# Kernel optimization log

Hardware: AMD Instinct MI355X
Metric: run time of the kernel (lower is better)

The kernel has to match this reference:

```python
import jax, jax.numpy as jnp
import numpy as np

B, T, E, H, DH = 8, 1024, 1024, 16, 64

def setup_inputs() -> dict:
    key = jax.random.key(0)
    ks = jax.random.split(key, 5)
    x = jax.random.normal(ks[0], (B, T, E), dtype=jnp.float32)
    Wq = jax.random.normal(ks[1], (H, E, DH), dtype=jnp.float32) * (E ** -0.5)
    Wk = jax.random.normal(ks[2], (H, E, DH), dtype=jnp.float32) * (E ** -0.5)
    Wv = jax.random.normal(ks[3], (H, E, DH), dtype=jnp.float32) * (E ** -0.5)
    Wp = jax.random.normal(ks[4], (E, E), dtype=jnp.float32) * (E ** -0.5)
    bp = jnp.zeros((E,), dtype=jnp.float32)
    return {"x": x, "Wq": Wq, "Wk": Wk, "Wv": Wv, "Wp": Wp, "bp": bp}

def reference(x, Wq, Wk, Wv, Wp, bp):
    # per-head projections (bias-free), vectorized over heads
    q = jnp.einsum('bte,hed->bhtd', x, Wq)
    k = jnp.einsum('bte,hed->bhtd', x, Wk)
    v = jnp.einsum('bte,hed->bhtd', x, Wv)
    scale = DH ** -0.5
    att = jnp.einsum('bhtd,bhsd->bhts', q, k) * scale  # [B,H,T,T]
    causal = jnp.tril(jnp.ones((T, T), dtype=bool))
    att = jnp.where(causal, att, -jnp.inf)
    att = jax.nn.softmax(att, axis=-1)
    # dropout is identity in eval mode
    out = jnp.einsum('bhts,bhsd->bhtd', att, v)
    out = out.transpose(0, 2, 1, 3).reshape(B, T, E)  # concat heads in order
    # proj: torch Linear y = x @ W^T + b
    out = out @ Wp.T + bp
    return out
```

## Files before the change

### kernel.cpp

```cpp
#include <hip/hip_runtime.h>

#define Bsz 8
#define Tsz 1024
#define Esz 1024
#define Hsz 16
#define DHsz 64
#define NQKV 3072

typedef _Float16 f16x8 __attribute__((ext_vector_type(8)));
typedef float f32x4 __attribute__((ext_vector_type(4)));
typedef unsigned short u16x8 __attribute__((ext_vector_type(8)));

__device__ __forceinline__ unsigned short f2h(float f) {
    union { _Float16 h; unsigned short u; } cv;
    cv.h = (_Float16)f;
    return cv.u;
}

__device__ __forceinline__ void async16(const void* g, void* l) {
    __builtin_amdgcn_global_load_lds(
        (const __attribute__((address_space(1))) void*)g,
        (__attribute__((address_space(3))) void*)l, 16, 0, 0);
}

#define MFMA(a, b, c) __builtin_amdgcn_mfma_f32_16x16x32_f16((a), (b), (c), 0, 0, 0)


__global__ void cast_f16_kernel(const float* __restrict__ in, unsigned short* __restrict__ outp) {
    int i = (blockIdx.x * 256 + threadIdx.x) * 4;
    float4 v = *(const float4*)(in + i);
    ushort4 o;
    o.x = f2h(v.x); o.y = f2h(v.y); o.z = f2h(v.z); o.w = f2h(v.w);
    *(ushort4*)(outp + i) = o;
}

__global__ void pack_wqkv_kernel(const float* __restrict__ Wq, const float* __restrict__ Wk,
                                 const float* __restrict__ Wv, unsigned short* __restrict__ Bt) {
    int i = (blockIdx.x * 256 + threadIdx.x) * 4;
    int n = i >> 10;
    int e = i & 1023;
    int which = n >> 10, rem = n & 1023, h = rem >> 6, d = rem & 63;
    const float* W = (which == 0) ? Wq : ((which == 1) ? Wk : Wv);
    const float* src = W + ((size_t)h * Esz + e) * DHsz + d;
    ushort4 o;
    o.x = f2h(src[0]);
    o.y = f2h(src[DHsz]);
    o.z = f2h(src[2 * DHsz]);
    o.w = f2h(src[3 * DHsz]);
    *(ushort4*)(Bt + i) = o;
}

__global__ __launch_bounds__(256) void vtrans_kernel(const unsigned short* __restrict__ QKV,
                                                     unsigned short* __restrict__ VT) {
    __shared__ unsigned int tile[64 * 33];
    const int bh = blockIdx.x, tc = blockIdx.y;
    const int b = bh >> 4, h = bh & 15;
    const int tid = threadIdx.x;
    const unsigned short* src = QKV + ((size_t)(b * Tsz) + tc * 64) * NQKV + 2048 + h * 64;
#pragma unroll
    for (int it = 0; it < 2; ++it) {
        int task = tid + it * 256;
        int row = task >> 3, seg = task & 7;
        u16x8 v = *(const u16x8*)(src + (size_t)row * NQKV + seg * 8);
#pragma unroll
        for (int jj = 0; jj < 4; ++jj)
            tile[row * 33 + seg * 4 + jj] =
                (unsigned int)v[2 * jj] | ((unsigned int)v[2 * jj + 1] << 16);
    }
    __syncthreads();
    unsigned short* dst = VT + (size_t)bh * DHsz * Tsz + tc * 64;
#pragma unroll
    for (int it = 0; it < 2; ++it) {
        int task = tid + it * 256;
        int d = task & 63, tseg = task >> 6;
        int du = d >> 1, hi = d & 1;
        u16x8 v;
#pragma unroll
        for (int j = 0; j < 8; ++j) {
            unsigned int w = tile[(tseg * 8 + j) * 33 + du];
            v[j] = (unsigned short)(hi ? (w >> 16) : (w & 0xffffu));
        }
        *(u16x8*)(dst + (size_t)d * Tsz + tseg * 8) = v;
    }
}

template <int MODE>
__global__ __launch_bounds__(256, 3) void gemm_bt(
    const unsigned short* __restrict__ A,
    const unsigned short* __restrict__ Bt,
    int K, int N,
    unsigned short* __restrict__ c16,
    float* __restrict__ outp, const float* __restrict__ bias)
{
    __shared__ unsigned short smem[17408];
    unsigned short* sA = smem;
    unsigned short* sB = smem + 4096;
    const int tid = threadIdx.x;
    const int wid = tid >> 6, lane = tid & 63;
    const int quad = lane >> 4, l16 = lane & 15;
    const int col0 = blockIdx.x * 128;
    const int row0 = blockIdx.y * 128;
    const int wm = (wid >> 1) * 64, wn = (wid & 1) * 64;

    const f32x4 zero4 = {0.f, 0.f, 0.f, 0.f};
    f32x4 acc[4][4];
#pragma unroll
    for (int i = 0; i < 4; ++i)
#pragma unroll
        for (int j = 0; j < 4; ++j) acc[i][j] = zero4;

    const unsigned short* gA = A + (size_t)row0 * K;
    const unsigned short* gB = Bt + (size_t)col0 * K;
    const int c0 = wid * 2;
    const int srw = lane >> 2;
    const int ssg = (lane & 3) * 8;

    for (int k0 = 0; k0 < K; k0 += 32) {
#pragma unroll
        for (int cc = 0; cc < 2; ++cc) {
            int c = c0 + cc;
            async16(gA + (size_t)(c * 16 + srw) * K + k0 + ssg, (void*)(sA + c * 512 + lane * 8));
            async16(gB + (size_t)(c * 16 + srw) * K + k0 + ssg, (void*)(sB + c * 512 + lane * 8));
        }
        __syncthreads();

        f16x8 af[4], bfr[4];
#pragma unroll
        for (int i = 0; i < 4; ++i)
            af[i] = *(const f16x8*)(sA + (wm + i * 16 + l16) * 32 + quad * 8);
#pragma unroll
        for (int j = 0; j < 4; ++j)
            bfr[j] = *(const f16x8*)(sB + (wn + j * 16 + l16) * 32 + quad * 8);
#pragma unroll
        for (int i = 0; i < 4; ++i)
#pragma unroll
            for (int j = 0; j < 4; ++j)
                acc[i][j] = MFMA(af[i], bfr[j], acc[i][j]);
        __syncthreads();
    }

    if (MODE == 0) {
#pragma unroll
        for (int i = 0; i < 4; ++i)
#pragma unroll
            for (int r = 0; r < 4; ++r) {
                int rowL = wm + i * 16 + quad * 4 + r;
                unsigned short* tr = smem + rowL * 136 + wn + l16;
#pragma unroll
                for (int j = 0; j < 4; ++j)
                    tr[j * 16] = f2h(acc[i][j][r]);
            }
        __syncthreads();
        unsigned short* ob = c16 + (size_t)row0 * N + col0;
#pragma unroll
        for (int it = 0; it < 8; ++it) {
            int rowG = wid * 32 + it * 4 + quad;
            u16x8 v = *(const u16x8*)(smem + rowG * 136 + l16 * 8);
            *(u16x8*)(ob + (size_t)rowG * N + l16 * 8) = v;
        }
    } else {
#pragma unroll
        for (int i = 0; i < 4; ++i) {
            int rb = row0 + wm + i * 16 + quad * 4;
#pragma unroll
            for (int r = 0; r < 4; ++r) {
                float* orow = outp + (size_t)(rb + r) * N;
#pragma unroll
                for (int j = 0; j < 4; ++j) {
                    int c = col0 + wn + j * 16 + l16;
                    orow[c] = acc[i][j][r] + bias[c];
                }
            }
        }
    }
}

__global__ __launch_bounds__(256, 4) void attn_kernel(
    const unsigned short* __restrict__ QKV,
    const unsigned short* __restrict__ VTg,
    unsigned short* __restrict__ AO)
{
    const int bh = blockIdx.x;
    const int qt = 7 - blockIdx.y;
    const int b = bh >> 4, h = bh & 15;
    const int q0 = qt * 128;
    const int tid = threadIdx.x, wid = tid >> 6, lane = tid & 63;
    const int quad = lane >> 4, l16 = lane & 15;

    __shared__ unsigned short sK[64 * 64];
    __shared__ unsigned short sVt[64 * 64];
    __shared__ unsigned short sP[128 * 72];

    const unsigned short* Qb = QKV + (size_t)(b * Tsz) * NQKV + h * 64;
    const unsigned short* Kb = QKV + (size_t)(b * Tsz) * NQKV + 1024 + h * 64;
    const unsigned short* VTb = VTg + (size_t)bh * DHsz * Tsz;

    const int srow = lane >> 3;
    const int sseg = lane & 7;
    const int slog = sseg ^ srow;

    const float C1 = 0.18033688f;
    const float C2 = -4.32808512f;
    const f32x4 zero4 = {0.f, 0.f, 0.f, 0.f};

    const int rowlo = q0 + wid * 32;
    const int prow0 = wid * 32;

    f16x8 qf[2][2];
#pragma unroll
    for (int rt = 0; rt < 2; ++rt)
#pragma unroll
        for (int kk = 0; kk < 2; ++kk)
            qf[rt][kk] = *(const f16x8*)(Qb + (size_t)(rowlo + rt * 16 + l16) * NQKV +
                                         kk * 32 + quad * 8);

    f32x4 o[2][4];
    float lp[2][4];
#pragma unroll
    for (int rt = 0; rt < 2; ++rt) {
#pragma unroll
        for (int dt = 0; dt < 4; ++dt) o[rt][dt] = zero4;
#pragma unroll
        for (int r = 0; r < 4; ++r) lp[rt][r] = 0.f;
    }

    const int nblk = (q0 >> 6) + 2;
    for (int blk = 0; blk < nblk; ++blk) {
        const int s0 = blk * 64;
        __syncthreads();
        {
            const int r0 = wid * 16;
#pragma unroll
            for (int ii = 0; ii < 2; ++ii) {
                int rr = r0 + ii * 8;
                async16(Kb + (size_t)(s0 + rr + srow) * NQKV + slog * 8,
                        (void*)(sK + rr * 64 + lane * 8));
                async16(VTb + (size_t)(rr + srow) * Tsz + s0 + slog * 8,
                        (void*)(sVt + rr * 64 + lane * 8));
            }
        }
        __syncthreads();

        if (s0 > rowlo + 31) continue;

        f32x4 sc[2][4];
#pragma unroll
        for (int rt = 0; rt < 2; ++rt)
#pragma unroll
            for (int ct = 0; ct < 4; ++ct) sc[rt][ct] = zero4;
#pragma unroll
        for (int kk = 0; kk < 2; ++kk) {
            f16x8 kf[4];
#pragma unroll
            for (int ct = 0; ct < 4; ++ct)
                kf[ct] = *(const f16x8*)(sK + (ct * 16 + l16) * 64 +
                                         (((kk * 4 + quad) ^ (l16 & 7)) * 8));
#pragma unroll
            for (int rt = 0; rt < 2; ++rt)
#pragma unroll
                for (int ct = 0; ct < 4; ++ct)
                    sc[rt][ct] = MFMA(qf[rt][kk], kf[ct], sc[rt][ct]);
        }

        if (s0 + 63 <= rowlo) {
#pragma unroll
            for (int rt = 0; rt < 2; ++rt)
#pragma unroll
                for (int r = 0; r < 4; ++r) {
                    unsigned short* pr = sP + (prow0 + rt * 16 + quad * 4 + r) * 72 + l16;
#pragma unroll
                    for (int ct = 0; ct < 4; ++ct) {
                        float p = exp2f(fmaf(sc[rt][ct][r], C1, C2));
                        lp[rt][r] += p;
                        pr[ct * 16] = f2h(p);
                    }
                }
        } else {
#pragma unroll
            for (int rt = 0; rt < 2; ++rt)
#pragma unroll
                for (int r = 0; r < 4; ++r) {
                    int qrow = rowlo + rt * 16 + quad * 4 + r;
                    unsigned short* pr = sP + (prow0 + rt * 16 + quad * 4 + r) * 72 + l16;
#pragma unroll
                    for (int ct = 0; ct < 4; ++ct) {
                        float p = exp2f(fmaf(sc[rt][ct][r], C1, C2));
                        p = (s0 + ct * 16 + l16 > qrow) ? 0.f : p;
                        lp[rt][r] += p;
                        pr[ct * 16] = f2h(p);
                    }
                }
        }

#pragma unroll
        for (int kk = 0; kk < 2; ++kk) {
            f16x8 pf[2], vf[4];
#pragma unroll
            for (int rt = 0; rt < 2; ++rt)
                pf[rt] = *(const f16x8*)(sP + (prow0 + rt * 16 + l16) * 72 +
                                         kk * 32 + quad * 8);
#pragma unroll
            for (int dt = 0; dt < 4; ++dt)
                vf[dt] = *(const f16x8*)(sVt + (dt * 16 + l16) * 64 +
                                         (((kk * 4 + quad) ^ (l16 & 7)) * 8));
#pragma unroll
            for (int rt = 0; rt < 2; ++rt)
#pragma unroll
                for (int dt = 0; dt < 4; ++dt)
                    o[rt][dt] = MFMA(pf[rt], vf[dt], o[rt][dt]);
        }
    }

#pragma unroll
    for (int rt = 0; rt < 2; ++rt)
#pragma unroll
        for (int r = 0; r < 4; ++r) {
            float s = lp[rt][r];
            s += __shfl_xor(s, 1, 64);
            s += __shfl_xor(s, 2, 64);
            s += __shfl_xor(s, 4, 64);
            s += __shfl_xor(s, 8, 64);
            float inv = 1.0f / s;
            int t = rowlo + rt * 16 + quad * 4 + r;
            size_t base = ((size_t)(b * Tsz + t)) * Esz + h * DHsz;
#pragma unroll
            for (int dt = 0; dt < 4; ++dt)
                AO[base + dt * 16 + l16] = f2h(o[rt][dt][r] * inv);
        }
}


extern "C" void kernel_launch(void* const* d_in, const int* in_sizes, int n_in,
                              void* d_out, int out_size, void* d_ws, size_t ws_size,
                              hipStream_t stream)
{
    const float* x  = (const float*)d_in[0];
    const float* Wq = (const float*)d_in[1];
    const float* Wk = (const float*)d_in[2];
    const float* Wv = (const float*)d_in[3];
    const float* Wp = (const float*)d_in[4];
    const float* bp = (const float*)d_in[5];
    float* out = (float*)d_out;

    char* ws = (char*)d_ws;
    unsigned short* xb   = (unsigned short*)(ws);
    unsigned short* wqkv = (unsigned short*)(ws + 16777216);
    unsigned short* wpb  = (unsigned short*)(ws + 23068672);
    unsigned short* qkv  = (unsigned short*)(ws + 25165824);
    unsigned short* ao   = (unsigned short*)(ws + 75497472);
    unsigned short* vtb  = xb;

    cast_f16_kernel<<<8192, 256, 0, stream>>>(x, xb);
    pack_wqkv_kernel<<<3072, 256, 0, stream>>>(Wq, Wk, Wv, wqkv);
    cast_f16_kernel<<<1024, 256, 0, stream>>>(Wp, wpb);

    gemm_bt<0><<<dim3(24, 64), 256, 0, stream>>>(xb, wqkv, 1024, 3072,
                                                 qkv, nullptr, nullptr);

    vtrans_kernel<<<dim3(128, 16), 256, 0, stream>>>(qkv, vtb);

    attn_kernel<<<dim3(128, 8), 256, 0, stream>>>(qkv, vtb, ao);

    gemm_bt<1><<<dim3(8, 64), 256, 0, stream>>>(ao, wpb, 1024, 1024,
                                                nullptr, out, bp);
}
```

Before: 294.8 us.

## Pair causal query tiles per block with 8 waves and staged output stores

The attention kernel now launches 512-thread blocks, and each block processes a pair of query tiles (7-p and p) one after the other, so every block does a balanced amount of causal work. Each wave now owns 16 query rows instead of 32, which lowers per-wave register use but halves the reuse of each K/V fragment loaded from LDS. The output tile is staged through shared memory and written with 16-byte vector stores instead of scattered 2-byte stores. The trade-offs are fewer blocks in total and twice as many block-wide barriers per block.

```diff
diff --git a/kernel.cpp b/kernel.cpp
--- a/kernel.cpp
+++ b/kernel.cpp
@@ -175,15 +175,14 @@
     }
 }
 
-__global__ __launch_bounds__(256, 4) void attn_kernel(
+__global__ __launch_bounds__(512, 4) void attn_kernel(
     const unsigned short* __restrict__ QKV,
     const unsigned short* __restrict__ VTg,
     unsigned short* __restrict__ AO)
 {
     const int bh = blockIdx.x;
-    const int qt = 7 - blockIdx.y;
+    const int pair = blockIdx.y;
     const int b = bh >> 4, h = bh & 15;
-    const int q0 = qt * 128;
     const int tid = threadIdx.x, wid = tid >> 6, lane = tid & 63;
     const int quad = lane >> 4, l16 = lane & 15;
 
@@ -198,135 +197,118 @@
     const int srow = lane >> 3;
     const int sseg = lane & 7;
     const int slog = sseg ^ srow;
+    const int r0 = wid * 8;
 
     const float C1 = 0.18033688f;
     const float C2 = -4.32808512f;
     const f32x4 zero4 = {0.f, 0.f, 0.f, 0.f};
 
-    const int rowlo = q0 + wid * 32;
-    const int prow0 = wid * 32;
-
-    f16x8 qf[2][2];
-#pragma unroll
-    for (int rt = 0; rt < 2; ++rt)
+    for (int half = 0; half < 2; ++half) {
+        const int qt = (half == 0) ? (7 - pair) : pair;
+        const int q0 = qt * 128;
+        const int rowlo = q0 + wid * 16;
+        const int prow0 = wid * 16;
+
+        f16x8 qf[2];
 #pragma unroll
         for (int kk = 0; kk < 2; ++kk)
-            qf[rt][kk] = *(const f16x8*)(Qb + (size_t)(rowlo + rt * 16 + l16) * NQKV +
-                                         kk * 32 + quad * 8);
-
-    f32x4 o[2][4];
-    float lp[2][4];
-#pragma unroll
-    for (int rt = 0; rt < 2; ++rt) {
-#pragma unroll
-        for (int dt = 0; dt < 4; ++dt) o[rt][dt] = zero4;
-#pragma unroll
-        for (int r = 0; r < 4; ++r) lp[rt][r] = 0.f;
-    }
-
-    const int nblk = (q0 >> 6) + 2;
-    for (int blk = 0; blk < nblk; ++blk) {
-        const int s0 = blk * 64;
-        __syncthreads();
-        {
-            const int r0 = wid * 16;
-#pragma unroll
-            for (int ii = 0; ii < 2; ++ii) {
-                int rr = r0 + ii * 8;
-                async16(Kb + (size_t)(s0 + rr + srow) * NQKV + slog * 8,
-                        (void*)(sK + rr * 64 + lane * 8));
-                async16(VTb + (size_t)(rr + srow) * Tsz + s0 + slog * 8,
-                        (void*)(sVt + rr * 64 + lane * 8));
-            }
-        }
-        __syncthreads();
-
-        if (s0 > rowlo + 31) continue;
-
-        f32x4 sc[2][4];
-#pragma unroll
-        for (int rt = 0; rt < 2; ++rt)
-#pragma unroll
-            for (int ct = 0; ct < 4; ++ct) sc[rt][ct] = zero4;
-#pragma unroll
-        for (int kk = 0; kk < 2; ++kk) {
-            f16x8 kf[4];
-#pragma unroll
-            for (int ct = 0; ct < 4; ++ct)
-                kf[ct] = *(const f16x8*)(sK + (ct * 16 + l16) * 64 +
-                                         (((kk * 4 + quad) ^ (l16 & 7)) * 8));
-#pragma unroll
-            for (int rt = 0; rt < 2; ++rt)
+            qf[kk] = *(const f16x8*)(Qb + (size_t)(rowlo + l16) * NQKV + kk * 32 + quad * 8);
+
+        f32x4 o[4];
+        float lp[4];
+#pragma unroll
+        for (int dt = 0; dt < 4; ++dt) o[dt] = zero4;
+#pragma unroll
+        for (int r = 0; r < 4; ++r) lp[r] = 0.f;
+
+        const int nblk = (q0 >> 6) + 2;
+        for (int blk = 0; blk < nblk; ++blk) {
+            const int s0 = blk * 64;
+            __syncthreads();
+            async16(Kb + (size_t)(s0 + r0 + srow) * NQKV + slog * 8,
+                    (void*)(sK + r0 * 64 + lane * 8));
+            async16(VTb + (size_t)(r0 + srow) * Tsz + s0 + slog * 8,
+                    (void*)(sVt + r0 * 64 + lane * 8));
+            __syncthreads();
+
+            if (s0 > rowlo + 15) continue;
+
+            f32x4 sc[4];
+#pragma unroll
+            for (int ct = 0; ct < 4; ++ct) sc[ct] = zero4;
+#pragma unroll
+            for (int kk = 0; kk < 2; ++kk) {
+                f16x8 kf[4];
 #pragma unroll
                 for (int ct = 0; ct < 4; ++ct)
-                    sc[rt][ct] = MFMA(qf[rt][kk], kf[ct], sc[rt][ct]);
-        }
-
-        if (s0 + 63 <= rowlo) {
-#pragma unroll
-            for (int rt = 0; rt < 2; ++rt)
+                    kf[ct] = *(const f16x8*)(sK + (ct * 16 + l16) * 64 +
+                                             (((kk * 4 + quad) ^ (l16 & 7)) * 8));
+#pragma unroll
+                for (int ct = 0; ct < 4; ++ct)
+                    sc[ct] = MFMA(qf[kk], kf[ct], sc[ct]);
+            }
+
+            if (s0 + 63 <= rowlo) {
 #pragma unroll
                 for (int r = 0; r < 4; ++r) {
-                    unsigned short* pr = sP + (prow0 + rt * 16 + quad * 4 + r) * 72 + l16;
+                    unsigned short* pr = sP + (prow0 + quad * 4 + r) * 72 + l16;
 #pragma unroll
                     for (int ct = 0; ct < 4; ++ct) {
-                        float p = exp2f(fmaf(sc[rt][ct][r], C1, C2));
-                        lp[rt][r] += p;
+                        float p = exp2f(fmaf(sc[ct][r], C1, C2));
+                        lp[r] += p;
                         pr[ct * 16] = f2h(p);
                     }
                 }
-        } else {
-#pragma unroll
-            for (int rt = 0; rt < 2; ++rt)
+            } else {
 #pragma unroll
                 for (int r = 0; r < 4; ++r) {
-                    int qrow = rowlo + rt * 16 + quad * 4 + r;
-                    unsigned short* pr = sP + (prow0 + rt * 16 + quad * 4 + r) * 72 + l16;
+                    int qrow = rowlo + quad * 4 + r;
+                    unsigned short* pr = sP + (prow0 + quad * 4 + r) * 72 + l16;
 #pragma unroll
                     for (int ct = 0; ct < 4; ++ct) {
-                        float p = exp2f(fmaf(sc[rt][ct][r], C1, C2));
+                        float p = exp2f(fmaf(sc[ct][r], C1, C2));
                         p = (s0 + ct * 16 + l16 > qrow) ? 0.f : p;
-                        lp[rt][r] += p;
+                        lp[r] += p;
                         pr[ct * 16] = f2h(p);
                     }
                 }
-        }
-
-#pragma unroll
-        for (int kk = 0; kk < 2; ++kk) {
-            f16x8 pf[2], vf[4];
-#pragma unroll
-            for (int rt = 0; rt < 2; ++rt)
-                pf[rt] = *(const f16x8*)(sP + (prow0 + rt * 16 + l16) * 72 +
-                                         kk * 32 + quad * 8);
-#pragma unroll
-            for (int dt = 0; dt < 4; ++dt)
-                vf[dt] = *(const f16x8*)(sVt + (dt * 16 + l16) * 64 +
-                                         (((kk * 4 + quad) ^ (l16 & 7)) * 8));
-#pragma unroll
-            for (int rt = 0; rt < 2; ++rt)
+            }
+
+#pragma unroll
+            for (int kk = 0; kk < 2; ++kk) {
+                f16x8 pf, vf[4];
+                pf = *(const f16x8*)(sP + (prow0 + l16) * 72 + kk * 32 + quad * 8);
 #pragma unroll
                 for (int dt = 0; dt < 4; ++dt)
-                    o[rt][dt] = MFMA(pf[rt], vf[dt], o[rt][dt]);
-        }
-    }
-
-#pragma unroll
-    for (int rt = 0; rt < 2; ++rt)
+                    vf[dt] = *(const f16x8*)(sVt + (dt * 16 + l16) * 64 +
+                                             (((kk * 4 + quad) ^ (l16 & 7)) * 8));
+#pragma unroll
+                for (int dt = 0; dt < 4; ++dt)
+                    o[dt] = MFMA(pf, vf[dt], o[dt]);
+            }
+        }
+
 #pragma unroll
         for (int r = 0; r < 4; ++r) {
-            float s = lp[rt][r];
+            float s = lp[r];
             s += __shfl_xor(s, 1, 64);
             s += __shfl_xor(s, 2, 64);
             s += __shfl_xor(s, 4, 64);
             s += __shfl_xor(s, 8, 64);
             float inv = 1.0f / s;
-            int t = rowlo + rt * 16 + quad * 4 + r;
-            size_t base = ((size_t)(b * Tsz + t)) * Esz + h * DHsz;
+            unsigned short* orow = sP + (prow0 + quad * 4 + r) * 72 + l16;
 #pragma unroll
             for (int dt = 0; dt < 4; ++dt)
-                AO[base + dt * 16 + l16] = f2h(o[rt][dt][r] * inv);
-        }
+                orow[dt * 16] = f2h(o[dt][r] * inv);
+        }
+#pragma unroll
+        for (int it = 0; it < 2; ++it) {
+            int r8 = it * 8 + srow;
+            u16x8 v = *(const u16x8*)(sP + (prow0 + r8) * 72 + sseg * 8);
+            *(u16x8*)(AO + ((size_t)(b * Tsz + q0 + wid * 16 + r8)) * Esz +
+                      h * 64 + sseg * 8) = v;
+        }
+    }
 }
 
 
@@ -359,7 +341,7 @@
 
     vtrans_kernel<<<dim3(128, 16), 256, 0, stream>>>(qkv, vtb);
 
-    attn_kernel<<<dim3(128, 8), 256, 0, stream>>>(qkv, vtb, ao);
+    attn_kernel<<<dim3(128, 4), 512, 0, stream>>>(qkv, vtb, ao);
 
     gemm_bt<1><<<dim3(8, 64), 256, 0, stream>>>(ao, wpb, 1024, 1024,
                                                 nullptr, out, bp);
```

Measured after the change: 257.3 us. 1.15x faster.
